# Optimization experiments

Hardware: AMD Instinct MI355X
Metric: run time of the kernel (lower is better)

The kernel has to match this reference:

```python
import jax, jax.numpy as jnp
import numpy as np

P = 256        # number of graph pairs
LMAX = 32      # max graph size (padded to LMAX+1 incl. virtual node)
F = 2048       # num_input_features
E = 256        # embedding_dim
INF = 10000.0


def _lengths():
    i = np.arange(P)
    len_s = 8 + (i % 25)
    len_t = 8 + ((7 * i + 3) % 25)
    return len_s.astype(np.int32), len_t.astype(np.int32)


def setup_inputs() -> dict:
    key = jax.random.key(0)
    ks = jax.random.split(key, 6)
    len_s_np, len_t_np = _lengths()
    Ns, Nt = int(len_s_np.sum()), int(len_t_np.sum())
    x_s = jax.random.normal(ks[0], (Ns, F), jnp.float32)
    x_t = jax.random.normal(ks[1], (Nt, F), jnp.float32)
    W1 = jax.random.normal(ks[2], (E, F), jnp.float32) / np.float32(np.sqrt(F))
    b1 = jnp.zeros((E,), jnp.float32)
    W2 = jax.random.normal(ks[3], (E, E), jnp.float32) / np.float32(np.sqrt(E))
    b2 = jnp.zeros((E,), jnp.float32)
    virtual_embedding = jax.random.uniform(ks[4], (F,), jnp.float32)
    return {"x_s": x_s, "x_t": x_t, "W1": W1, "b1": b1, "W2": W2, "b2": b2,
            "virtual_embedding": virtual_embedding,
            "len_s": jnp.asarray(len_s_np), "len_t": jnp.asarray(len_t_np)}


def _embed(x, W1, b1, W2, b2):
    # nn.Sequential(Linear, Dropout(eval=identity), ReLU, Linear, ReLU)
    h = jax.nn.relu(x @ W1.T + b1)
    return jax.nn.relu(h @ W2.T + b2)


def _safe_cdist(a, b):
    # a: [P,L,E], b: [P,L,E] -> [P,L,L] Euclidean, grad-safe at 0
    sq = (jnp.sum(a * a, -1)[:, :, None] + jnp.sum(b * b, -1)[:, None, :]
          - 2.0 * jnp.einsum('pid,pjd->pij', a, b))
    sq = jnp.maximum(sq, 0.0)
    pos = sq > 0
    return jnp.where(pos, jnp.sqrt(jnp.where(pos, sq, 1.0)), 0.0)


def _pad_embed(emb, virtual_e, lens):
    # ragged [N,E] -> padded [P,LMAX+1,E]; slot lens[p] (and beyond) = virtual
    pos = jnp.arange(LMAX + 1)
    off = jnp.cumsum(lens) - lens                       # exclusive prefix sum
    idx = off[:, None] + jnp.minimum(pos[None, :], lens[:, None] - 1)
    mask = pos[None, :] < lens[:, None]
    return jnp.where(mask[..., None], emb[idx], virtual_e[None, None, :])


def _edit_costs(x_s, x_t, W1, b1, W2, b2, virtual_embedding, len_s, len_t):
    emb_s = _embed(x_s, W1, b1, W2, b2)
    emb_t = _embed(x_t, W1, b1, W2, b2)
    ve = _embed(virtual_embedding[None, :], W1, b1, W2, b2)[0]
    A = _pad_embed(emb_s, ve, len_s)                    # [P,L+1,E]
    B = _pad_embed(emb_t, ve, len_t)
    d = _safe_cdist(A, B)                               # [P,L+1,L+1]
    pos = jnp.arange(LMAX + 1)
    valid = ((pos[None, :, None] <= len_s[:, None, None]) &
             (pos[None, None, :] <= len_t[:, None, None]))
    tot = jnp.sum(jnp.where(valid, d, 0.0), axis=(1, 2))
    scale = (len_s * len_t).astype(d.dtype) / tot
    return jnp.where(valid, d * scale[:, None, None], 0.0), valid


def _lap_jv(C):
    # Jonker-Volgenant / e-maxx Hungarian for square cost matrix; returns col of each row
    C = np.asarray(C, dtype=np.float64)
    n = C.shape[0]
    u = np.zeros(n + 1)
    v = np.zeros(n + 1)
    p = np.zeros(n + 1, dtype=np.int64)
    way = np.zeros(n + 1, dtype=np.int64)
    for i in range(1, n + 1):
        p[0] = i
        j0 = 0
        minv = np.full(n + 1, np.inf)
        used = np.zeros(n + 1, dtype=bool)
        while True:
            used[j0] = True
            i0 = p[j0]
            cur = C[i0 - 1, :] - u[i0] - v[1:]
            upd = (~used[1:]) & (cur < minv[1:])
            minv[1:][upd] = cur[upd]
            way[1:][upd] = j0
            masked = np.where(used[1:], np.inf, minv[1:])
            j1 = int(np.argmin(masked)) + 1
            delta = masked[j1 - 1]
            u[p[used]] += delta
            v[used] -= delta
            minv[1:][~used[1:]] -= delta
            j0 = j1
            if p[j0] == 0:
                break
        while j0:
            j1 = way[j0]
            p[j0] = p[j1]
            j0 = j1
    row_of_col = p[1:] - 1
    col_of_row = np.empty(n, dtype=np.int64)
    col_of_row[row_of_col] = np.arange(n)
    return col_of_row


def _lsape_align(ec, n, m):
    # LSAPE expansion identical to GEDModelHomology.lsape
    N = n + m
    C = np.zeros((N, N))
    C[:n, :m] = ec[:n, :m]
    C[n:, :m] = INF
    C[:n, m:] = INF
    C[np.arange(n, n + m), np.arange(m)] = ec[n, :m]
    C[np.arange(n), np.arange(m, m + n)] = ec[:n, m]
    C[~np.isfinite(C)] = INF
    p = _lap_jv(C)
    q = np.arange(N)
    align = np.zeros((n + 1, m + 1), dtype=np.int32)
    align[np.minimum(q, n), np.minimum(p, m)] = 1
    align[-1, -1] = 0
    return align


def _alignments(costs_np, len_s_np, len_t_np):
    out = np.zeros((costs_np.shape[0], LMAX + 1, LMAX + 1), dtype=np.int32)
    for pr in range(costs_np.shape[0]):
        n, m = int(len_s_np[pr]), int(len_t_np[pr])
        out[pr, :n + 1, :m + 1] = _lsape_align(costs_np[pr, :n + 1, :m + 1], n, m)
    return out


def reference(x_s, x_t, W1, b1, W2, b2, virtual_embedding, len_s, len_t):
    costs, _ = _edit_costs(x_s, x_t, W1, b1, W2, b2, virtual_embedding, len_s, len_t)
    aligns = jnp.asarray(_alignments(np.asarray(costs),
                                     np.asarray(len_s), np.asarray(len_t)))
    geds = (jnp.sum(aligns.astype(costs.dtype) * costs, axis=(1, 2))
            / (len_s + len_t).astype(costs.dtype))
    return aligns, costs, geds
```

## Files before the change

### kernel.cpp

```cpp
#include <hip/hip_runtime.h>
#include <math.h>

#define LMAXP1 33
#define EDIM   256
#define FBIG   3.0e38f

typedef _Float16 half8 __attribute__((ext_vector_type(8)));
typedef float    f32x4 __attribute__((ext_vector_type(4)));

__device__ inline unsigned pk2h(_Float16 a, _Float16 b) {
    union { _Float16 h[2]; unsigned u; } q; q.h[0] = a; q.h[1] = b; return q.u;
}

__global__ __launch_bounds__(256)
void k_convw(const float* __restrict__ W, unsigned* __restrict__ Wh,
             unsigned* __restrict__ Wl, int npairs, float scale) {
    const int stride = gridDim.x * blockDim.x;
    for (int i = blockIdx.x * blockDim.x + threadIdx.x; i < npairs; i += stride) {
        const float a0 = W[2*i] * scale, a1 = W[2*i+1] * scale;
        const _Float16 h0 = (_Float16)a0, h1 = (_Float16)a1;
        const _Float16 l0 = (_Float16)(a0 - (float)h0);
        const _Float16 l1 = (_Float16)(a1 - (float)h1);
        Wh[i] = pk2h(h0, h1); Wl[i] = pk2h(l0, l1);
    }
}

__global__ __launch_bounds__(256)
void k_norms(const unsigned* __restrict__ Eh, const unsigned* __restrict__ El,
             float* __restrict__ Norms, int Mtot) {
    const int row  = blockIdx.x * 4 + (threadIdx.x >> 6);
    const int lane = threadIdx.x & 63;
    if (row >= Mtot) return;
    const uint2 h2 = *(const uint2*)(Eh + (size_t)row * 128 + lane * 2);
    const uint2 l2 = *(const uint2*)(El + (size_t)row * 128 + lane * 2);
    union { unsigned u; _Float16 h[2]; } qh, ql;
    float s = 0.f;
    qh.u = h2.x; ql.u = l2.x;
    { const float x0 = (float)qh.h[0] + (float)ql.h[0];
      const float x1 = (float)qh.h[1] + (float)ql.h[1];
      s = fmaf(x0, x0, s); s = fmaf(x1, x1, s); }
    qh.u = h2.y; ql.u = l2.y;
    { const float x0 = (float)qh.h[0] + (float)ql.h[0];
      const float x1 = (float)qh.h[1] + (float)ql.h[1];
      s = fmaf(x0, x0, s); s = fmaf(x1, x1, s); }
    #pragma unroll
    for (int off = 32; off > 0; off >>= 1) s += __shfl_xor(s, off);
    if (lane == 0) Norms[row] = s;
}

#define ASTR 20
__global__ __launch_bounds__(256)
void k_gemm_splitk(const float* __restrict__ S0, int n0,
                   const float* __restrict__ S1, int n1,
                   const float* __restrict__ S2,
                   const unsigned* __restrict__ Wh, const unsigned* __restrict__ Wl,
                   float* __restrict__ Part, int Mtot, int K, int kchunk) {
    __shared__ alignas(16) unsigned AsH[64 * ASTR],  AsL[64 * ASTR];
    __shared__ alignas(16) unsigned BsH[256 * ASTR], BsL[256 * ASTR];
    const int tid = threadIdx.x;
    const int m0  = blockIdx.x * 64;
    const int ks  = blockIdx.z;
    const int kb  = ks * kchunk;
    const int ke  = (kb + kchunk < K) ? kb + kchunk : K;

    const int sar = tid >> 2, sak = (tid & 3) << 3;
    const int gr  = m0 + sar;
    const float* srow = nullptr;
    if (gr < n0)            srow = S0 + (size_t)gr * K;
    else if (gr < n0 + n1)  srow = S1 + (size_t)(gr - n0) * K;
    else if (gr < Mtot)     srow = S2;

    const int lane = tid & 63, wv = tid >> 6;
    const int wc = wv << 6;
    const int lr = lane & 15, lq = lane >> 4;

    f32x4 acc[4][4] = {};

    for (int k0 = kb; k0 < ke; k0 += 32) {
        {
            float x[8];
            if (srow) {
                const float4 f0 = *(const float4*)(srow + k0 + sak + 0);
                const float4 f1 = *(const float4*)(srow + k0 + sak + 4);
                x[0]=f0.x; x[1]=f0.y; x[2]=f0.z; x[3]=f0.w;
                x[4]=f1.x; x[5]=f1.y; x[6]=f1.z; x[7]=f1.w;
            } else {
                #pragma unroll
                for (int j = 0; j < 8; ++j) x[j] = 0.f;
            }
            unsigned uh[4], ul[4];
            #pragma unroll
            for (int j = 0; j < 4; ++j) {
                const _Float16 h0 = (_Float16)x[2*j],   h1 = (_Float16)x[2*j+1];
                const _Float16 l0 = (_Float16)(x[2*j]   - (float)h0);
                const _Float16 l1 = (_Float16)(x[2*j+1] - (float)h1);
                uh[j] = pk2h(h0, h1); ul[j] = pk2h(l0, l1);
            }
            *(uint4*)(AsH + sar * ASTR + (sak >> 1)) = make_uint4(uh[0],uh[1],uh[2],uh[3]);
            *(uint4*)(AsL + sar * ASTR + (sak >> 1)) = make_uint4(ul[0],ul[1],ul[2],ul[3]);
        }
        #pragma unroll
        for (int it = 0; it < 4; ++it) {
            const int idx = tid + it * 256;
            const int br = idx >> 2, bk = (idx & 3) << 3;
            const size_t uoff = (size_t)br * (K >> 1) + ((k0 + bk) >> 1);
            *(uint4*)(BsH + br * ASTR + (bk >> 1)) = *(const uint4*)(Wh + uoff);
            *(uint4*)(BsL + br * ASTR + (bk >> 1)) = *(const uint4*)(Wl + uoff);
        }
        __syncthreads();

        half8 bhv[4], blv[4];
        #pragma unroll
        for (int ct = 0; ct < 4; ++ct) {
            const int br = wc + ct * 16 + lr;
            bhv[ct] = *(const half8*)((const char*)BsH + br * 80 + lq * 16);
            blv[ct] = *(const half8*)((const char*)BsL + br * 80 + lq * 16);
        }
        #pragma unroll
        for (int rt = 0; rt < 4; ++rt) {
            const int ar = rt * 16 + lr;
            const half8 ah = *(const half8*)((const char*)AsH + ar * 80 + lq * 16);
            const half8 al = *(const half8*)((const char*)AsL + ar * 80 + lq * 16);
            #pragma unroll
            for (int ct = 0; ct < 4; ++ct) {
                acc[rt][ct] = __builtin_amdgcn_mfma_f32_16x16x32_f16(ah, bhv[ct], acc[rt][ct], 0, 0, 0);
                acc[rt][ct] = __builtin_amdgcn_mfma_f32_16x16x32_f16(ah, blv[ct], acc[rt][ct], 0, 0, 0);
                acc[rt][ct] = __builtin_amdgcn_mfma_f32_16x16x32_f16(al, bhv[ct], acc[rt][ct], 0, 0, 0);
            }
        }
        __syncthreads();
    }

    float* pout = Part + (size_t)ks * ((size_t)Mtot * EDIM);
    const float sc = 1.0f / 1024.0f;
    #pragma unroll
    for (int rt = 0; rt < 4; ++rt) {
        #pragma unroll
        for (int r = 0; r < 4; ++r) {
            const int grr = m0 + rt * 16 + lq * 4 + r;
            if (grr >= Mtot) continue;
            #pragma unroll
            for (int ct = 0; ct < 4; ++ct)
                pout[(size_t)grr * EDIM + wc + ct * 16 + lr] = acc[rt][ct][r] * sc;
        }
    }
}

__global__ __launch_bounds__(256)
void k_reduce_bias_relu(const float* __restrict__ Part,
                        const float* __restrict__ bias,
                        unsigned* __restrict__ Hh, unsigned* __restrict__ Hl,
                        int S, size_t MN4) {
    const size_t i = (size_t)blockIdx.x * blockDim.x + threadIdx.x;
    const size_t stride = (size_t)gridDim.x * blockDim.x;
    const size_t MN = MN4 * 4;
    for (size_t i4 = i; i4 < MN4; i4 += stride) {
        float4 s = ((const float4*)Part)[i4];
        for (int z = 1; z < S; ++z)
            { const float4 q = ((const float4*)(Part + (size_t)z * MN))[i4];
              s.x += q.x; s.y += q.y; s.z += q.z; s.w += q.w; }
        const float4 b = ((const float4*)bias)[i4 & 63];
        s.x = fmaxf(s.x + b.x, 0.f); s.y = fmaxf(s.y + b.y, 0.f);
        s.z = fmaxf(s.z + b.z, 0.f); s.w = fmaxf(s.w + b.w, 0.f);
        const _Float16 hx = (_Float16)s.x, hy = (_Float16)s.y;
        const _Float16 hz = (_Float16)s.z, hw = (_Float16)s.w;
        Hh[i4*2+0] = pk2h(hx, hy);
        Hh[i4*2+1] = pk2h(hz, hw);
        Hl[i4*2+0] = pk2h((_Float16)(s.x - (float)hx), (_Float16)(s.y - (float)hy));
        Hl[i4*2+1] = pk2h((_Float16)(s.z - (float)hz), (_Float16)(s.w - (float)hw));
    }
}

__global__ __launch_bounds__(256)
void k_gemm_f16(const unsigned* __restrict__ Ah, const unsigned* __restrict__ Al,
                const unsigned* __restrict__ Wh, const unsigned* __restrict__ Wl,
                const float* __restrict__ bias,
                unsigned* __restrict__ Eh, unsigned* __restrict__ El,
                int Mtot, int K) {
    __shared__ alignas(16) unsigned AsH[64 * ASTR],  AsL[64 * ASTR];
    __shared__ alignas(16) unsigned BsH[256 * ASTR], BsL[256 * ASTR];
    const int tid = threadIdx.x;
    const int m0  = blockIdx.x * 64;

    const int sar = tid >> 2, sak = (tid & 3) << 3;
    const int gr  = m0 + sar;
    const bool arow = (gr < Mtot);

    const int lane = tid & 63, wv = tid >> 6;
    const int wc = wv << 6;
    const int lr = lane & 15, lq = lane >> 4;

    f32x4 acc[4][4] = {};

    for (int k0 = 0; k0 < K; k0 += 32) {
        {
            uint4 vh = make_uint4(0,0,0,0), vl = vh;
            if (arow) {
                const size_t uoff = (size_t)gr * (K >> 1) + ((k0 + sak) >> 1);
                vh = *(const uint4*)(Ah + uoff);
                vl = *(const uint4*)(Al + uoff);
            }
            *(uint4*)(AsH + sar * ASTR + (sak >> 1)) = vh;
            *(uint4*)(AsL + sar * ASTR + (sak >> 1)) = vl;
        }
        #pragma unroll
        for (int it = 0; it < 4; ++it) {
            const int idx = tid + it * 256;
            const int br = idx >> 2, bk = (idx & 3) << 3;
            const size_t uoff = (size_t)br * (K >> 1) + ((k0 + bk) >> 1);
            *(uint4*)(BsH + br * ASTR + (bk >> 1)) = *(const uint4*)(Wh + uoff);
            *(uint4*)(BsL + br * ASTR + (bk >> 1)) = *(const uint4*)(Wl + uoff);
        }
        __syncthreads();

        half8 bhv[4], blv[4];
        #pragma unroll
        for (int ct = 0; ct < 4; ++ct) {
            const int br = wc + ct * 16 + lr;
            bhv[ct] = *(const half8*)((const char*)BsH + br * 80 + lq * 16);
            blv[ct] = *(const half8*)((const char*)BsL + br * 80 + lq * 16);
        }
        #pragma unroll
        for (int rt = 0; rt < 4; ++rt) {
            const int ar = rt * 16 + lr;
            const half8 ah = *(const half8*)((const char*)AsH + ar * 80 + lq * 16);
            const half8 al = *(const half8*)((const char*)AsL + ar * 80 + lq * 16);
            #pragma unroll
            for (int ct = 0; ct < 4; ++ct) {
                acc[rt][ct] = __builtin_amdgcn_mfma_f32_16x16x32_f16(ah, bhv[ct], acc[rt][ct], 0, 0, 0);
                acc[rt][ct] = __builtin_amdgcn_mfma_f32_16x16x32_f16(ah, blv[ct], acc[rt][ct], 0, 0, 0);
                acc[rt][ct] = __builtin_amdgcn_mfma_f32_16x16x32_f16(al, bhv[ct], acc[rt][ct], 0, 0, 0);
            }
        }
        __syncthreads();
    }

    _Float16* ph = (_Float16*)Eh;
    _Float16* pl = (_Float16*)El;
    const float sc = 1.0f / 1024.0f;
    #pragma unroll
    for (int rt = 0; rt < 4; ++rt) {
        #pragma unroll
        for (int r = 0; r < 4; ++r) {
            const int grr = m0 + rt * 16 + lq * 4 + r;
            if (grr >= Mtot) continue;
            #pragma unroll
            for (int ct = 0; ct < 4; ++ct) {
                const int gc = wc + ct * 16 + lr;
                const float vv = fmaxf(acc[rt][ct][r] * sc + bias[gc], 0.0f);
                const _Float16 hv = (_Float16)vv;
                ph[(size_t)grr * EDIM + gc] = hv;
                pl[(size_t)grr * EDIM + gc] = (_Float16)(vv - (float)hv);
            }
        }
    }
}

__global__ __launch_bounds__(256)
void k_embed_gemm(const float* __restrict__ S0, int n0,
                  const float* __restrict__ S1, int n1,
                  const float* __restrict__ S2,
                  const float* __restrict__ W, const float* __restrict__ bias,
                  float* __restrict__ C, int Mtot, int K) {
    __shared__ alignas(16) float As[16][68];
    __shared__ alignas(16) float Bs[16][68];
    const int tid  = threadIdx.x;
    const int tx   = tid & 15, ty = tid >> 4;
    const int m0   = blockIdx.x * 64, nc0 = blockIdx.y * 64;
    const int lrow = tid >> 2;
    const int lk4  = (tid & 3) << 2;

    const int gr = m0 + lrow;
    const float* srow = nullptr;
    if (gr < n0)            srow = S0 + (size_t)gr * K;
    else if (gr < n0 + n1)  srow = S1 + (size_t)(gr - n0) * K;
    else if (gr < Mtot)     srow = S2;
    const float* wrow = W + (size_t)(nc0 + lrow) * K;

    float acc[4][4] = {};
    for (int k0 = 0; k0 < K; k0 += 16) {
        float4 va = make_float4(0.f, 0.f, 0.f, 0.f);
        if (srow) va = *(const float4*)(srow + k0 + lk4);
        const float4 vb = *(const float4*)(wrow + k0 + lk4);
        As[lk4+0][lrow] = va.x; As[lk4+1][lrow] = va.y;
        As[lk4+2][lrow] = va.z; As[lk4+3][lrow] = va.w;
        Bs[lk4+0][lrow] = vb.x; Bs[lk4+1][lrow] = vb.y;
        Bs[lk4+2][lrow] = vb.z; Bs[lk4+3][lrow] = vb.w;
        __syncthreads();
        #pragma unroll
        for (int kk = 0; kk < 16; ++kk) {
            const float4 a4 = *(const float4*)&As[kk][ty << 2];
            const float4 b4 = *(const float4*)&Bs[kk][tx << 2];
            const float av[4] = {a4.x, a4.y, a4.z, a4.w};
            const float bv[4] = {b4.x, b4.y, b4.z, b4.w};
            #pragma unroll
            for (int i2 = 0; i2 < 4; ++i2)
                #pragma unroll
                for (int j2 = 0; j2 < 4; ++j2)
                    acc[i2][j2] = fmaf(av[i2], bv[j2], acc[i2][j2]);
        }
        __syncthreads();
    }
    #pragma unroll
    for (int i2 = 0; i2 < 4; ++i2) {
        const int grr = m0 + (ty << 2) + i2;
        if (grr >= Mtot) continue;
        #pragma unroll
        for (int j2 = 0; j2 < 4; ++j2) {
            const int gc = nc0 + (tx << 2) + j2;
            const float vv = acc[i2][j2] + bias[gc];
            C[(size_t)grr * EDIM + gc] = fmaxf(vv, 0.0f);
        }
    }
}

#define CSTR 36
__global__ __launch_bounds__(256)
void k_costs(const unsigned* __restrict__ Eh, const unsigned* __restrict__ El,
             const float* __restrict__ Norms,
             const int* __restrict__ len_s, const int* __restrict__ len_t,
             int Ns, int Nt, float* __restrict__ costs) {
    __shared__ alignas(16) unsigned Ah[34 * CSTR], Al[34 * CSTR];
    __shared__ alignas(16) unsigned Bh[34 * CSTR], Bl[34 * CSTR];
    __shared__ float dtile[LMAXP1 * LMAXP1];
    __shared__ float na[LMAXP1], nb[LMAXP1];
    __shared__ float red[256];
    __shared__ float s_scale;
    const int p = blockIdx.x, tid = threadIdx.x;
    const int n = len_s[p], m = len_t[p];
    int offs = 0, offt = 0;
    for (int j = 0; j < p; ++j) { offs += len_s[j]; offt += len_t[j]; }
    const int veRow = Ns + Nt;
    const int tbase = Ns + offt;

    const int lane = tid & 63, wv = tid >> 6;
    const int lr = lane & 15, lq = lane >> 4;

    if (tid <= n)                       na[tid] = Norms[(tid < n) ? offs + tid : veRow];
    else if (tid >= 64 && tid - 64 <= m) nb[tid - 64] = Norms[(tid - 64 < m) ? tbase + tid - 64 : veRow];

    f32x4 g0 = {}, g1 = {}, g2 = {};
    const int t0 = wv, t1 = wv + 4, t2 = wv + 8;

    for (int k0 = 0; k0 < EDIM; k0 += 64) {
        for (int idx = tid; idx < 34 * 16; idx += 256) {
            const int r = idx >> 4, c4 = idx & 15;
            const int rowA = (r < n) ? offs + r : ((r == n) ? veRow : -1);
            const int rowB = (r < m) ? tbase + r : ((r == m) ? veRow : -1);
            uint2 vah = make_uint2(0,0), val = vah, vbh = vah, vbl = vah;
            if (rowA >= 0) {
                const size_t uo_ = (size_t)rowA * 128 + (k0 >> 1) + c4 * 2;
                vah = *(const uint2*)(Eh + uo_); val = *(const uint2*)(El + uo_);
            }
            if (rowB >= 0) {
                const size_t uo_ = (size_t)rowB * 128 + (k0 >> 1) + c4 * 2;
                vbh = *(const uint2*)(Eh + uo_); vbl = *(const uint2*)(El + uo_);
            }
            const int uo = r * CSTR + c4 * 2;
            *(uint2*)(Ah + uo) = vah; *(uint2*)(Al + uo) = val;
            *(uint2*)(Bh + uo) = vbh; *(uint2*)(Bl + uo) = vbl;
        }
        __syncthreads();

        #pragma unroll
        for (int kf = 0; kf < 2; ++kf) {
#define GRAM_TILE(T, G) { \
            const int tr_ = (T) / 3, tc_ = (T) % 3;                              \
            const int ar_ = tr_ * 16 + lr, br_ = tc_ * 16 + lr;                  \
            const half8 ah = *(const half8*)((const char*)Ah + ar_*144 + kf*64 + lq*16); \
            const half8 al = *(const half8*)((const char*)Al + ar_*144 + kf*64 + lq*16); \
            const half8 bh = *(const half8*)((const char*)Bh + br_*144 + kf*64 + lq*16); \
            const half8 bl = *(const half8*)((const char*)Bl + br_*144 + kf*64 + lq*16); \
            G = __builtin_amdgcn_mfma_f32_16x16x32_f16(ah, bh, G, 0, 0, 0);      \
            G = __builtin_amdgcn_mfma_f32_16x16x32_f16(ah, bl, G, 0, 0, 0);      \
            G = __builtin_amdgcn_mfma_f32_16x16x32_f16(al, bh, G, 0, 0, 0); }
            GRAM_TILE(t0, g0)
            GRAM_TILE(t1, g1)
            if (wv == 0) GRAM_TILE(t2, g2)
#undef GRAM_TILE
        }
        __syncthreads();
    }

#define DTILE_OUT(T, G) { \
    const int tr_ = (T) / 3, tc_ = (T) % 3;                                      \
    _Pragma("unroll")                                                            \
    for (int r = 0; r < 4; ++r) {                                                \
        const int i_ = tr_ * 16 + lq * 4 + r, j_ = tc_ * 16 + lr;                \
        if (i_ <= n && j_ <= m) {                                                \
            const float sq = fmaxf(na[i_] + nb[j_] - 2.0f * G[r], 0.0f);         \
            dtile[i_ * LMAXP1 + j_] = (sq > 0.0f) ? sqrtf(sq) : 0.0f;            \
        } } }
    DTILE_OUT(t0, g0)
    DTILE_OUT(t1, g1)
    if (wv == 0) DTILE_OUT(t2, g2)
#undef DTILE_OUT
    __syncthreads();

    float lsum = 0.f;
    const int m1 = m + 1;
    const int cells = (n + 1) * m1;
    for (int c = tid; c < cells; c += 256) {
        const int i = c / m1, j = c - i * m1;
        lsum += dtile[i * LMAXP1 + j];
    }
    red[tid] = lsum;
    __syncthreads();
    for (int s = 128; s > 0; s >>= 1) {
        if (tid < s) red[tid] += red[tid + s];
        __syncthreads();
    }
    if (tid == 0) s_scale = (float)(n * m) / red[0];
    __syncthreads();
    const float scale = s_scale;
    for (int idx = tid; idx < LMAXP1 * LMAXP1; idx += 256) {
        const int i = idx / LMAXP1, j = idx - i * LMAXP1;
        const float v = (i <= n && j <= m) ? dtile[i * LMAXP1 + j] * scale : 0.0f;
        costs[(size_t)p * (LMAXP1 * LMAXP1) + idx] = v;
    }
}

__device__ inline int rdlane_i(int v, int l) { return __builtin_amdgcn_readlane(v, l); }
__device__ inline float rdlane_f(float v, int l) {
    return __int_as_float(__builtin_amdgcn_readlane(__float_as_int(v), l));
}
__device__ inline unsigned wave_umin64(unsigned x) {
#define DPPMINU(ctrl) { unsigned t_ = (unsigned)__builtin_amdgcn_update_dpp(  \
        (int)x, (int)x, (ctrl), 0xf, 0xf, false);                             \
        x = (t_ < x) ? t_ : x; }
    DPPMINU(0xB1)
    DPPMINU(0x4E)
    DPPMINU(0x141)
    DPPMINU(0x140)
    DPPMINU(0x142)
    DPPMINU(0x143)
#undef DPPMINU
    return (unsigned)__builtin_amdgcn_readlane((int)x, 63);
}

__global__ __launch_bounds__(64)
void k_lap(const float* __restrict__ costs, const int* __restrict__ len_s,
           const int* __restrict__ len_t, float* __restrict__ aligns,
           float* __restrict__ geds) {
    __shared__ float ec[LMAXP1 * LMAXP1];
    __shared__ float Ms[33 * 64];
    const int p = blockIdx.x, lane = threadIdx.x;
    const int n = len_s[p], m = len_t[p];
    const float* cp = costs + (size_t)p * (LMAXP1 * LMAXP1);
    for (int idx = lane; idx < LMAXP1 * LMAXP1; idx += 64) ec[idx] = cp[idx];
    __syncthreads();

    const bool swp = (n > m);
    const int R  = swp ? n : m;
    const int S_ = swp ? m : n;
    const bool vec = (lane >= 1 && lane <= R);

    for (int r = 1; r <= R; ++r) {
        float cv = FBIG;
        const int i0b = r - 1, j0b = lane - 1;
        if (vec) {
            if (!swp) {
                const float ins = ec[n * LMAXP1 + j0b];
                cv = (i0b < S_)
                   ? fminf(ec[i0b * LMAXP1 + j0b], ec[i0b * LMAXP1 + m] + ins)
                   : ins;
            } else {
                const float ins = ec[j0b * LMAXP1 + m];
                cv = (i0b < S_)
                   ? fminf(ec[j0b * LMAXP1 + i0b], ec[n * LMAXP1 + i0b] + ins)
                   : ins;
            }
        }
        Ms[(r << 6) + lane] = cv;
    }
    __syncthreads();

    float v_l = 0.0f;
    int amin_l = 0;
    if (vec) {
        float best = FBIG;
        for (int r = 1; r <= R; ++r) {
            const float c = Ms[(r << 6) + lane];
            if (c < best) { best = c; amin_l = r; }
        }
        v_l = best;
    }
    int p_l = 0;
    unsigned long long rowfree = ((1ull << R) - 1ull) << 1;
    for (int j = 1; j <= R; ++j) {
        const int ai = rdlane_i(amin_l, j);
        if ((rowfree >> ai) & 1ull) {
            if (lane == j) p_l = ai;
            rowfree &= ~(1ull << ai);
        }
    }

    float ucol = 0.0f, minv_l = FBIG;
    int way_l = 0;

    for (int i = 1; i <= R; ++i) {
        if (!((rowfree >> i) & 1ull)) continue;
        if (lane == 0) { p_l = i; ucol = 0.0f; }
        minv_l = FBIG;
        int used_l = 0;
        int j0 = 0, i0 = i;
        float u_i0 = 0.0f;
        while (true) {
            if (lane == j0) used_l = 1;
            const float cur = Ms[(i0 << 6) + lane] - u_i0 - v_l;
            const bool unused = vec && !used_l;
            if (unused && cur < minv_l) { minv_l = cur; way_l = j0; }
            const float mval = unused ? fmaxf(minv_l, 0.0f) : FBIG;
            const unsigned key = (__float_as_uint(mval) & ~63u) | (unsigned)lane;
            const unsigned kmin = wave_umin64(key);
            const int j1 = (int)(kmin & 63u);
            const float delta = rdlane_f(minv_l, j1);
            if (used_l) { ucol += delta; v_l -= delta; }
            if (unused) minv_l -= delta;
            j0 = j1;
            i0 = rdlane_i(p_l, j1);
            u_i0 = rdlane_f(ucol, j1);
            if (i0 == 0) break;
        }
        int jj = j0;
        while (jj != 0) {
            const int   j1a = rdlane_i(way_l, jj);
            const int   pn  = rdlane_i(p_l, j1a);
            const float un  = rdlane_f(ucol, j1a);
            if (lane == jj) { p_l = pn; ucol = un; }
            jj = j1a;
        }
    }

    float* ap = aligns + (size_t)p * (LMAXP1 * LMAXP1);
    for (int idx = lane; idx < LMAXP1 * LMAXP1; idx += 64) ap[idx] = 0.0f;
    __syncthreads();
    float gedv = 0.0f;
    if (vec) {
        const int i0b = p_l - 1;
        const int j0b = lane - 1;
        if (!swp) {
            if (i0b < S_) {
                const float sub = ec[i0b * LMAXP1 + j0b];
                const float alt = ec[i0b * LMAXP1 + m] + ec[n * LMAXP1 + j0b];
                if (sub <= alt) { ap[i0b * LMAXP1 + j0b] = 1.0f; gedv = sub; }
                else { ap[i0b * LMAXP1 + m] = 1.0f;
                       ap[n * LMAXP1 + j0b] = 1.0f;
                       gedv = alt; }
            } else {
                ap[n * LMAXP1 + j0b] = 1.0f;
                gedv = ec[n * LMAXP1 + j0b];
            }
        } else {
            if (i0b < S_) {
                const float sub = ec[j0b * LMAXP1 + i0b];
                const float alt = ec[n * LMAXP1 + i0b] + ec[j0b * LMAXP1 + m];
                if (sub <= alt) { ap[j0b * LMAXP1 + i0b] = 1.0f; gedv = sub; }
                else { ap[n * LMAXP1 + i0b] = 1.0f;
                       ap[j0b * LMAXP1 + m] = 1.0f;
                       gedv = alt; }
            } else {
                ap[j0b * LMAXP1 + m] = 1.0f;
                gedv = ec[j0b * LMAXP1 + m];
            }
        }
    }
    #pragma unroll
    for (int off = 32; off > 0; off >>= 1) gedv += __shfl_xor(gedv, off);
    if (lane == 0) geds[p] = gedv / (float)(n + m);
}

extern "C" void kernel_launch(void* const* d_in, const int* in_sizes, int n_in,
                              void* d_out, int out_size, void* d_ws, size_t ws_size,
                              hipStream_t stream) {
    const float* x_s = (const float*)d_in[0];
    const float* x_t = (const float*)d_in[1];
    const float* W1  = (const float*)d_in[2];
    const float* b1  = (const float*)d_in[3];
    const float* W2  = (const float*)d_in[4];
    const float* b2  = (const float*)d_in[5];
    const float* ve  = (const float*)d_in[6];
    const int* len_s = (const int*)d_in[7];
    const int* len_t = (const int*)d_in[8];
    const int P    = in_sizes[7];
    const int Ns   = in_sizes[0] / 2048;
    const int Nt   = in_sizes[1] / 2048;
    const int Mtot = Ns + Nt + 1;
    const size_t MN  = (size_t)Mtot * EDIM;

    float* out_aligns = (float*)d_out;
    float* out_costs  = out_aligns + (size_t)P * LMAXP1 * LMAXP1;
    float* out_geds   = out_costs  + (size_t)P * LMAXP1 * LMAXP1;

    const dim3 b256(256);
    const int gx64 = (Mtot + 63) / 64;
    const int gnorm = (Mtot + 3) / 4;

    const size_t fixed = MN + 10240 + 2 * 262144 + 2 * 32768;
    int S = 0;
    if (ws_size >= (4 * MN + fixed) * sizeof(float)) S = 4;
    else if (ws_size >= (2 * MN + fixed) * sizeof(float)) S = 2;

    if (S > 0) {
        float* Part = (float*)d_ws;
        unsigned* Eh  = (unsigned*)Part;
        unsigned* El  = Eh + MN / 2;
        unsigned* Hh  = (unsigned*)(Part + (size_t)S * MN);
        unsigned* Hl  = Hh + MN / 2;
        float* Norms  = (float*)(Hl + MN / 2);
        unsigned* W1h = (unsigned*)(Norms + 10240);
        unsigned* W1l = W1h + 262144;
        unsigned* W2h = W1l + 262144;
        unsigned* W2l = W2h + 32768;

        k_convw<<<dim3(1024), b256, 0, stream>>>(W1, W1h, W1l, 262144, 1024.0f);
        k_convw<<<dim3(128),  b256, 0, stream>>>(W2, W2h, W2l, 32768, 1024.0f);

        k_gemm_splitk<<<dim3(gx64, 1, S), b256, 0, stream>>>(
            x_s, Ns, x_t, Nt, ve, W1h, W1l, Part, Mtot, 2048, 2048 / S);

        const size_t MN4 = MN / 4;
        const int rblocks = (int)((MN4 + 255) / 256) < 2048
                          ? (int)((MN4 + 255) / 256) : 2048;
        k_reduce_bias_relu<<<dim3(rblocks), b256, 0, stream>>>(Part, b1, Hh, Hl, S, MN4);

        k_gemm_f16<<<dim3(gx64), b256, 0, stream>>>(Hh, Hl, W2h, W2l, b2, Eh, El, Mtot, 256);
        k_norms<<<dim3(gnorm), b256, 0, stream>>>(Eh, El, Norms, Mtot);

        k_costs<<<dim3(P), b256, 0, stream>>>(Eh, El, Norms, len_s, len_t, Ns, Nt, out_costs);
        k_lap<<<dim3(P), dim3(64), 0, stream>>>(out_costs, len_s, len_t, out_aligns, out_geds);
    } else {
        float* H   = (float*)d_ws;
        float* Emb = H + MN;
        unsigned* Eh = (unsigned*)(Emb + MN);
        unsigned* El = Eh + MN / 2;
        float* Norms = (float*)(El + MN / 2);
        k_embed_gemm<<<dim3(gx64, 4), b256, 0, stream>>>(
            x_s, Ns, x_t, Nt, ve, W1, b1, H, Mtot, 2048);
        k_embed_gemm<<<dim3(gx64, 4), b256, 0, stream>>>(
            H, Mtot, nullptr, 0, nullptr, W2, b2, Emb, Mtot, 256);
        k_convw<<<dim3(1024), b256, 0, stream>>>(Emb, Eh, El, (int)(MN / 2), 1.0f);
        k_norms<<<dim3(gnorm), b256, 0, stream>>>(Eh, El, Norms, Mtot);
        k_costs<<<dim3(P), b256, 0, stream>>>(Eh, El, Norms, len_s, len_t, Ns, Nt, out_costs);
        k_lap<<<dim3(P), dim3(64), 0, stream>>>(out_costs, len_s, len_t, out_aligns, out_geds);
    }
}
```

Before: 177.0 us.

## Add augmenting row reduction pass before shortest-path LAP augmentation

Inserts a Jonker-Volgenant style augmenting row reduction phase between column reduction and the Dijkstra-style augmentation loop. Each free row finds its best and second-best reduced costs with wave-wide min reductions, claims the best column, and may displace that column's previous owner, which is requeued; the number of pops is capped at 3R. The aim is to assign most rows cheaply so fewer expensive shortest-path augmentations run, at the cost of extra wave reductions and some risk of changing tie-breaking between equal-cost optimal assignments.

After: 168.4 us. -4.9%, faster.

```diff
diff --git a/kernel.cpp b/kernel.cpp
--- a/kernel.cpp
+++ b/kernel.cpp
@@ -495,7 +495,43 @@
         }
     }
 
-    float ucol = 0.0f, minv_l = FBIG;
+    float ucol = 0.0f;
+    {
+        unsigned long long q = rowfree;
+        int pops = 0;
+        const int cap = 3 * R;
+        while (q && pops < cap) {
+            const int i = __ffsll(q) - 1;
+            q &= ~(1ull << i);
+            ++pops;
+            const float rc = vec ? fmaxf(Ms[(i << 6) + lane] - v_l, 0.0f) : FBIG;
+            const unsigned key = (__float_as_uint(rc) & ~63u) | (unsigned)lane;
+            const unsigned k1 = wave_umin64(key);
+            int j1 = (int)(k1 & 63u);
+            const float min1 = rdlane_f(rc, j1);
+            const unsigned key2 = (lane == j1) ? 0xFFFFFFFFu : key;
+            const unsigned k2 = wave_umin64(key2);
+            const float min2 = rdlane_f(rc, (int)(k2 & 63u));
+            int owner = rdlane_i(p_l, j1);
+            const bool strict = (min1 < min2);
+            if (!strict) {
+                const unsigned long long ball =
+                    __ballot(vec && (rc == min1) && (p_l == 0));
+                if (ball == 0ull) continue;
+                j1 = __ffsll(ball) - 1;
+                j1 = __builtin_amdgcn_readfirstlane(j1);
+                owner = 0;
+            }
+            if (lane == j1) {
+                p_l = i; ucol = min2;
+                if (strict) v_l -= (min2 - min1);
+            }
+            rowfree &= ~(1ull << i);
+            if (owner != 0) { rowfree |= (1ull << owner); q |= (1ull << owner); }
+        }
+    }
+
+    float minv_l = FBIG;
     int way_l = 0;
 
     for (int i = 1; i <= R; ++i) {
```
